# Optimization experiments

Hardware: AMD Instinct MI355X
Metric: run time of the kernel (lower is better)

The kernel has to match this reference:

```python
import jax, jax.numpy as jnp
import numpy as np

# dimensions
N = 50000    # nodes
E = 600000   # edges
NS = 64      # scalar (0e) channels of node features
NV = 32      # vector (1o) channels of node features
A = 16       # node attr channels (16x0e)
R = 8        # edge embedding dim (radial basis, 8x0e)
H = 8        # fc_hidden_size
AVG_NB = 12.0  # avg_num_neighbors
# gate layout: NS scalars (silu) + NV gate scalars (sigmoid) gating NV vectors
GS = NS + NV  # 96 scalar channels before gate
NW = NS + NS + NV + NV  # 192 per-edge TP weights (paths: s*Y0->0e, s*Y1->1o, v*Y0->1o, v.Y1->0e)


def setup_inputs() -> dict:
    key = jax.random.key(0)
    ks = jax.random.split(key, 20)
    d = {
        'node_s': jax.random.normal(ks[0], (N, NS), jnp.float32),
        'node_v': jax.random.normal(ks[1], (N, NV, 3), jnp.float32),
        'node_attrs': jax.random.normal(ks[2], (N, A), jnp.float32),
        'edge_emb': jax.random.uniform(ks[3], (E, R), jnp.float32),
        'edge_sh0': jnp.ones((E, 1), jnp.float32),
        'edge_sh1': jax.random.normal(ks[4], (E, 3), jnp.float32),
        'edge_index': jax.random.randint(ks[5], (2, E), 0, N),
        # linear_1 on node feats (per-irrep channel mixing)
        'W1s': jax.random.normal(ks[6], (NS, NS), jnp.float32),
        'W1v': jax.random.normal(ks[7], (NV, NV), jnp.float32),
        # radial MLP producing per-edge TP weights
        'Wm1': jax.random.normal(ks[8], (R, H), jnp.float32),
        'Wm2': jax.random.normal(ks[9], (H, NW), jnp.float32),
        # linear_2: TP out (96x0e+96x1o) -> pre-gate (96x0e+32x1o)
        'W2s': jax.random.normal(ks[10], (GS, GS), jnp.float32),
        'W2v': jax.random.normal(ks[11], (NS + NV, NV), jnp.float32),
        # update UVU TP internal weights (msg x attrs)
        'Wt0': jax.random.normal(ks[12], (NS, A), jnp.float32),
        'Wt1': jax.random.normal(ks[13], (NV, A), jnp.float32),
        # linear_3
        'W3s': jax.random.normal(ks[14], (NS, GS), jnp.float32),
        'W3v': jax.random.normal(ks[15], (NV, NV), jnp.float32),
        # self connection: FullyConnectedTensorProduct(node_feats, attrs -> pre-gate)
        'Wsc0': jax.random.normal(ks[16], (NS, A, GS), jnp.float32),
        'Wsc1': jax.random.normal(ks[17], (NV, A, NV), jnp.float32),
    }
    return d


def _gate(s_all, v):
    # s_all: [.., GS]; first NS scalars -> silu, last NV -> sigmoid gates for vectors
    scal = jax.nn.silu(s_all[..., :NS])
    gates = jax.nn.sigmoid(s_all[..., NS:])
    return scal, v * gates[..., None]


def reference(node_s, node_v, node_attrs, edge_emb, edge_sh0, edge_sh1, edge_index,
              W1s, W1v, Wm1, Wm2, W2s, W2v, Wt0, Wt1, W3s, W3v, Wsc0, Wsc1):
    src, dst = edge_index[0], edge_index[1]

    # ---- message ----
    s1 = (node_s @ W1s) / jnp.sqrt(jnp.float32(NS))                       # [N,NS]
    v1 = jnp.einsum('nuc,uv->nvc', node_v, W1v) / jnp.sqrt(jnp.float32(NV))
    ss = s1[src]   # [E,NS]
    vv = v1[src]   # [E,NV,3]

    # per-edge TP weights from radial MLP
    w = jax.nn.silu(edge_emb @ Wm1) @ Wm2                                 # [E,NW]
    w0a, w1a, w1b, w0b = jnp.split(w, [NS, 2 * NS, 2 * NS + NV], axis=1)

    # UVU tensor product with SH edge attrs (lmax=1)
    t0a = w0a * ss * edge_sh0                                             # [E,NS] 0e
    t0b = w0b * jnp.einsum('euc,ec->eu', vv, edge_sh1)                    # [E,NV] 0e
    t1a = w1a[:, :, None] * ss[:, :, None] * edge_sh1[:, None, :]         # [E,NS,3] 1o
    t1b = w1b[:, :, None] * vv * edge_sh0[:, :, None]                     # [E,NV,3] 1o
    tp_s = jnp.concatenate([t0a, t0b], axis=1)                            # [E,96]
    tp_v = jnp.concatenate([t1a, t1b], axis=1)                            # [E,96,3]

    m_s = (tp_s @ W2s) / jnp.sqrt(jnp.float32(GS))                        # [E,GS]
    m_v = jnp.einsum('euc,uv->evc', tp_v, W2v) / jnp.sqrt(jnp.float32(NS + NV))  # [E,NV,3]
    msg_s, msg_v = _gate(m_s, m_v)                                        # [E,NS], [E,NV,3]

    # ---- update ----
    agg_s = jax.ops.segment_sum(msg_s, dst, num_segments=N) / jnp.sqrt(jnp.float32(AVG_NB))
    agg_v = jax.ops.segment_sum(msg_v, dst, num_segments=N) / jnp.sqrt(jnp.float32(AVG_NB))

    u0 = jnp.einsum('nu,na,ua->nu', agg_s, node_attrs, Wt0) / jnp.sqrt(jnp.float32(A))
    u1 = jnp.einsum('nuc,na,ua->nuc', agg_v, node_attrs, Wt1) / jnp.sqrt(jnp.float32(A))

    f_s = (u0 @ W3s) / jnp.sqrt(jnp.float32(NS))                          # [N,GS]
    f_v = jnp.einsum('nuc,uv->nvc', u1, W3v) / jnp.sqrt(jnp.float32(NV))  # [N,NV,3]

    # self connection (fully connected TP with scalar attrs)
    sc_s = jnp.einsum('nu,na,uav->nv', node_s, node_attrs, Wsc0) / jnp.sqrt(jnp.float32(NS * A))
    sc_v = jnp.einsum('nuc,na,uaw->nwc', node_v, node_attrs, Wsc1) / jnp.sqrt(jnp.float32(NV * A))
    f_s = f_s + sc_s
    f_v = f_v + sc_v

    out_s, out_v = _gate(f_s, f_v)                                        # [N,NS], [N,NV,3]
    return jnp.concatenate([out_s, out_v.reshape(N, NV * 3)], axis=1)     # [N,160]
```

## Files before the change

### kernel.cpp

```cpp
#include <hip/hip_runtime.h>
#include <math.h>
#include <stdint.h>

#define N 50000
#define E 600000
#define EPB 16
#define LDK 104

typedef __attribute__((ext_vector_type(8))) short short8;
typedef __attribute__((ext_vector_type(4))) float float4v;

__device__ __forceinline__ float silu_f(float x) { return x / (1.f + __expf(-x)); }
__device__ __forceinline__ float sigm_f(float x) { return 1.f / (1.f + __expf(-x)); }
__device__ __forceinline__ unsigned short f2bf(float f) {
  unsigned u = __float_as_uint(f);
  u += 0x7fff + ((u >> 16) & 1);
  return (unsigned short)(u >> 16);
}
__device__ __forceinline__ float bf2f(unsigned short u) {
  return __uint_as_float(((unsigned)u) << 16);
}

__global__ void k_hist(const int* __restrict__ eidx, int* __restrict__ counts) {
  int e = blockIdx.x * 256 + threadIdx.x;
  if (e < E) atomicAdd(&counts[eidx[E + e]], 1);
}

__global__ __launch_bounds__(1024)
void k_scan(const int* __restrict__ counts, int* __restrict__ row_ptr) {
  __shared__ int ssum[1024];
  const int t = threadIdx.x;
  const int CH = 49;
  int lo = t * CH, hi = min(lo + CH, N);
  int s = 0;
  for (int i = lo; i < hi; i++) s += counts[i];
  ssum[t] = s;
  __syncthreads();
  for (int off = 1; off < 1024; off <<= 1) {
    int v = (t >= off) ? ssum[t - off] : 0;
    __syncthreads();
    ssum[t] += v;
    __syncthreads();
  }
  int run = (t == 0) ? 0 : ssum[t - 1];
  for (int i = lo; i < hi; i++) { row_ptr[i] = run; run += counts[i]; }
  if (t == 1023) row_ptr[N] = ssum[1023];
}

__global__ void k_scatter(const int* __restrict__ eidx, const int* __restrict__ row_ptr,
                          int* __restrict__ woff, int* __restrict__ perm) {
  int e = blockIdx.x * 256 + threadIdx.x;
  if (e < E) {
    int d = eidx[E + e];
    int p = atomicAdd(&woff[d], 1);
    perm[row_ptr[d] + p] = e;
  }
}

__global__ __launch_bounds__(256)
void k_init(const float* __restrict__ Wsc0, const float* __restrict__ W3s,
            const float* __restrict__ Wsc1, const float* __restrict__ W3v,
            const float* __restrict__ W2s, const float* __restrict__ W2v,
            unsigned short* __restrict__ BT, unsigned short* __restrict__ B2T,
            unsigned short* __restrict__ w2sTg, unsigned short* __restrict__ w2vTg,
            const float* __restrict__ node_s, const float* __restrict__ node_v,
            const float* __restrict__ W1s, const float* __restrict__ W1v,
            float* __restrict__ s1, float* __restrict__ v1,
            int* __restrict__ cnt, float* __restrict__ aggs) {
  __shared__ float w1s[64 * 64];
  __shared__ float w1v[32 * 32];
  const int b = blockIdx.x, t = threadIdx.x;
  const float isq96 = 0.10206207261596575f;

  if (b < 528) {
    int i = b * 256 + t;
    if (i < 96 * 1088) {
      int j = i / 1088, k = i % 1088;
      float v;
      if (k < 1024) v = Wsc0[(size_t)k * 96 + j] * 0.03125f;
      else          v = W3s[(size_t)(k - 1024) * 96 + j] * 0.125f;
      BT[i] = f2bf(v);
    } else if (i < 96 * 1088 + 32 * 576) {
      int i2 = i - 96 * 1088;
      int w = i2 / 576, k = i2 % 576;
      float v = 0.f;
      if (k < 512)      v = Wsc1[(size_t)k * 32 + w] * 0.04419417382415922f;
      else if (k < 544) v = W3v[(size_t)(k - 512) * 32 + w] * 0.17677669529663689f;
      B2T[i2] = f2bf(v);
    } else if (i < 96 * 1088 + 32 * 576 + 96 * 96) {
      int i3 = i - (96 * 1088 + 32 * 576);
      int j = i3 / 96, k = i3 % 96;
      w2sTg[i3] = f2bf(W2s[(size_t)k * 96 + j] * isq96);
    } else {
      int i4 = i - (96 * 1088 + 32 * 576 + 96 * 96);
      if (i4 < 32 * 96) {
        int v = i4 / 96, u = i4 % 96;
        w2vTg[i4] = f2bf(W2v[(size_t)u * 32 + v] * isq96);
      }
    }
  } else if (b < 1552) {
    for (int i = t; i < 64 * 64; i += 256) w1s[i] = W1s[i];
    for (int i = t; i < 32 * 32; i += 256) w1v[i] = W1v[i];
    __syncthreads();
    const float is_ns = 0.125f;
    const float is_nv = 0.17677669529663689f;
    int gtid = (b - 528) * 256 + t;
    const int stride = 1024 * 256;
    for (int i = gtid; i < N * 160; i += stride) {
      int n = i / 160, ch = i % 160;
      if (ch < 64) {
        const float* row = node_s + n * 64;
        float acc = 0.f;
#pragma unroll
        for (int u = 0; u < 64; u++) acc += row[u] * w1s[u * 64 + ch];
        s1[n * 64 + ch] = acc * is_ns;
      } else {
        int p = ch - 64, v = p / 3, c = p % 3;
        const float* row = node_v + n * 96;
        float acc = 0.f;
#pragma unroll
        for (int u = 0; u < 32; u++) acc += row[u * 3 + c] * w1v[u * 32 + v];
        v1[n * 96 + p] = acc * is_nv;
      }
    }
  } else if (b < 1943) {
    if (cnt) {
      int idx = (b - 1552) * 256 + t;
      if (idx < 2 * N) cnt[idx] = 0;
    }
  } else {
    float4v* a4 = (float4v*)aggs;
    const int tot = N * 160 / 4;
    const float4v z = {0.f, 0.f, 0.f, 0.f};
    for (int i = (b - 1943) * 256 + t; i < tot; i += 2000 * 256) a4[i] = z;
  }
}

template<int STORE>
__global__ __launch_bounds__(256, 4)
void k_msg(const float* __restrict__ s1, const float* __restrict__ v1,
           const float* __restrict__ emb, const float* __restrict__ sh0g,
           const float* __restrict__ sh1g, const int* __restrict__ eidx,
           const int* __restrict__ perm,
           const float* __restrict__ Wm1, const float* __restrict__ Wm2,
           const unsigned short* __restrict__ w2sTg, const unsigned short* __restrict__ w2vTg,
           float* __restrict__ aggs, float* __restrict__ aggv) {
  __shared__ float wm2s[192 * 9];
  __shared__ float wm1s[64];
  __shared__ unsigned short tps[EPB * LDK];
  __shared__ unsigned short tpv[EPB * 3 * LDK];
  __shared__ float gat[EPB][33];
  __shared__ float msL[EPB][65];
  __shared__ float mvL[EPB][97];
  __shared__ float hb[EPB][8];
  __shared__ float sh1b[EPB][4];
  __shared__ float sh0b[EPB];
  __shared__ int ssrc[EPB];
  __shared__ int sdst[EPB];

  const int t = threadIdx.x;
  const int wave = t >> 6, lane = t & 63;
  const int lm = lane & 15, quad = lane >> 4;
  const int subc = t & 15;

  for (int i = t; i < 192 * 8; i += 256) {
    int h = i / 192, c = i % 192;
    wm2s[c * 9 + h] = Wm2[i];
  }
  if (t < 64) wm1s[t] = Wm1[t];

  short8 b1fr[2][3], b2fr[3];
  {
    const int nt0 = wave;
    const int nt1 = (wave + 4 < 6) ? wave + 4 : wave;
    const int nv2 = wave & 1;
#pragma unroll
    for (int kk = 0; kk < 3; kk++) {
      b1fr[0][kk] = *(const short8*)&w2sTg[(nt0 * 16 + lm) * 96 + kk * 32 + quad * 8];
      b1fr[1][kk] = *(const short8*)&w2sTg[(nt1 * 16 + lm) * 96 + kk * 32 + quad * 8];
      b2fr[kk]    = *(const short8*)&w2vTg[(nv2 * 16 + lm) * 96 + kk * 32 + quad * 8];
    }
  }
  __syncthreads();

  for (int pass = blockIdx.x; pass < E / EPB; pass += gridDim.x) {
    const int ebase = pass * EPB;
    __syncthreads();
    if (t < EPB) {
      const int e = STORE ? perm[ebase + t] : (ebase + t);
      ssrc[t] = eidx[e];
      sdst[t] = eidx[E + e];
      sh0b[t] = sh0g[e];
    } else if (t >= 64 && t < 64 + EPB * 3) {
      int i = t - 64;
      const int el = i / 3, c = i % 3;
      const int e = STORE ? perm[ebase + el] : (ebase + el);
      sh1b[el][c] = sh1g[e * 3 + c];
    } else if (t >= 128) {
      int i = t - 128, el = i >> 3, sub = i & 7;
      const int e = STORE ? perm[ebase + el] : (ebase + el);
      float acc = 0.f;
#pragma unroll
      for (int r = 0; r < 8; r++) acc += emb[e * 8 + r] * wm1s[r * 8 + sub];
      hb[el][sub] = silu_f(acc);
    }
    __syncthreads();
    {
      const int el = t >> 4, sub = subc;
      const int src = ssrc[el];
      const float s0v = sh0b[el];
      const float x0 = sh1b[el][0], x1 = sh1b[el][1], x2 = sh1b[el][2];
      float hr[8];
#pragma unroll
      for (int h = 0; h < 8; h++) hr[h] = hb[el][h];
      const float4v ss = *(const float4v*)&s1[(size_t)src * 64 + sub * 4];
      unsigned short tsv[4], tvv[3][4];
#pragma unroll
      for (int i = 0; i < 4; i++) {
        float w0a = 0.f, w1a = 0.f;
#pragma unroll
        for (int h = 0; h < 8; h++) {
          w0a += hr[h] * wm2s[(sub * 4 + i) * 9 + h];
          w1a += hr[h] * wm2s[(64 + sub * 4 + i) * 9 + h];
        }
        const float ssu = ss[i];
        tsv[i] = f2bf(w0a * ssu * s0v);
        const float base = w1a * ssu;
        tvv[0][i] = f2bf(base * x0);
        tvv[1][i] = f2bf(base * x1);
        tvv[2][i] = f2bf(base * x2);
      }
      *(uint2*)&tps[el * LDK + sub * 4] = *(uint2*)tsv;
#pragma unroll
      for (int c = 0; c < 3; c++)
        *(uint2*)&tpv[(el * 3 + c) * LDK + sub * 4] = *(uint2*)tvv[c];
      const float2* vp = (const float2*)&v1[(size_t)src * 96 + sub * 6];
      const float2 va = vp[0], vb = vp[1], vc = vp[2];
      const float v6[6] = {va.x, va.y, vb.x, vb.y, vc.x, vc.y};
      unsigned short ts2[2], tv2[3][2];
#pragma unroll
      for (int i2 = 0; i2 < 2; i2++) {
        float w1b = 0.f, w0b = 0.f;
#pragma unroll
        for (int h = 0; h < 8; h++) {
          w1b += hr[h] * wm2s[(128 + sub * 2 + i2) * 9 + h];
          w0b += hr[h] * wm2s[(160 + sub * 2 + i2) * 9 + h];
        }
        const float vx = v6[i2 * 3 + 0], vy = v6[i2 * 3 + 1], vz = v6[i2 * 3 + 2];
        ts2[i2] = f2bf(w0b * (vx * x0 + vy * x1 + vz * x2));
        tv2[0][i2] = f2bf(w1b * vx * s0v);
        tv2[1][i2] = f2bf(w1b * vy * s0v);
        tv2[2][i2] = f2bf(w1b * vz * s0v);
      }
      *(unsigned*)&tps[el * LDK + 64 + sub * 2] = *(unsigned*)ts2;
#pragma unroll
      for (int c = 0; c < 3; c++)
        *(unsigned*)&tpv[(el * 3 + c) * LDK + 64 + sub * 2] = *(unsigned*)tv2[c];
    }
    __syncthreads();
    if (STORE) {
      short8 afr[3];
#pragma unroll
      for (int kk = 0; kk < 3; kk++)
        afr[kk] = *(const short8*)&tps[lm * LDK + kk * 32 + quad * 8];
#pragma unroll
      for (int tt = 0; tt < 3; tt++) {
        const int id = wave + tt * 4;
        float4v acc = {0.f, 0.f, 0.f, 0.f};
        if (id < 6) {
          const int t2 = id >> 2;
#pragma unroll
          for (int kk = 0; kk < 3; kk++)
            acc = __builtin_amdgcn_mfma_f32_16x16x32_bf16(afr[kk], b1fr[t2][kk], acc, 0, 0, 0);
          const int j = id * 16 + lm;
#pragma unroll
          for (int reg = 0; reg < 4; reg++) {
            const int e = quad * 4 + reg;
            const float val = acc[reg];
            if (j < 64) msL[e][j] = silu_f(val);
            else        gat[e][j - 64] = sigm_f(val);
          }
        } else {
          const int g2 = id - 6;
          const int mt = g2 >> 1, nt2 = g2 & 1;
#pragma unroll
          for (int kk = 0; kk < 3; kk++) {
            short8 a = *(const short8*)&tpv[(mt * 16 + lm) * LDK + kk * 32 + quad * 8];
            acc = __builtin_amdgcn_mfma_f32_16x16x32_bf16(a, b2fr[kk], acc, 0, 0, 0);
          }
          const int v = nt2 * 16 + lm;
#pragma unroll
          for (int reg = 0; reg < 4; reg++) {
            const int r = mt * 16 + quad * 4 + reg;
            const int e = (r * 171) >> 9, c = r - 3 * e;
            mvL[e][v * 3 + c] = acc[reg];
          }
        }
      }
      __syncthreads();
      if (t < 160) {
        const int col = t - 64;
        const int gv = (col * 171) >> 9;
        float acc = 0.f;
        int cur = sdst[0];
        for (int s2 = 0; s2 < EPB; s2++) {
          const int d = sdst[s2];
          const float val = (t < 64) ? msL[s2][t] : mvL[s2][col] * gat[s2][gv];
          if (d != cur) {
            if (t < 64) atomicAdd(&aggs[(size_t)cur * 64 + t], acc);
            else        atomicAdd(&aggv[(size_t)cur * 96 + col], acc);
            acc = 0.f; cur = d;
          }
          acc += val;
        }
        if (t < 64) atomicAdd(&aggs[(size_t)cur * 64 + t], acc);
        else        atomicAdd(&aggv[(size_t)cur * 96 + col], acc);
      }
    } else {
      {
        short8 afr[3];
#pragma unroll
        for (int kk = 0; kk < 3; kk++)
          afr[kk] = *(const short8*)&tps[lm * LDK + kk * 32 + quad * 8];
#pragma unroll
        for (int t2 = 0; t2 < 2; t2++) {
          const int nt = wave + t2 * 4;
          if (nt < 6) {
            float4v acc = {0.f, 0.f, 0.f, 0.f};
#pragma unroll
            for (int kk = 0; kk < 3; kk++)
              acc = __builtin_amdgcn_mfma_f32_16x16x32_bf16(afr[kk], b1fr[t2][kk], acc, 0, 0, 0);
            const int j = nt * 16 + lm;
#pragma unroll
            for (int reg = 0; reg < 4; reg++) {
              const int e = quad * 4 + reg;
              const float val = acc[reg];
              if (j < 64) atomicAdd(&aggs[(size_t)sdst[e] * 64 + j], silu_f(val));
              else        gat[e][j - 64] = sigm_f(val);
            }
          }
        }
      }
      __syncthreads();
#pragma unroll
      for (int t2 = 0; t2 < 2; t2++) {
        const int tile = wave + t2 * 4;
        if (tile < 6) {
          const int mt = tile >> 1, nt2 = tile & 1;
          float4v acc = {0.f, 0.f, 0.f, 0.f};
#pragma unroll
          for (int kk = 0; kk < 3; kk++) {
            short8 a = *(const short8*)&tpv[(mt * 16 + lm) * LDK + kk * 32 + quad * 8];
            acc = __builtin_amdgcn_mfma_f32_16x16x32_bf16(a, b2fr[kk], acc, 0, 0, 0);
          }
          const int v = nt2 * 16 + lm;
#pragma unroll
          for (int reg = 0; reg < 4; reg++) {
            const int r = mt * 16 + quad * 4 + reg;
            const int e = (r * 171) >> 9, c = r - 3 * e;
            atomicAdd(&aggv[(size_t)sdst[e] * 96 + v * 3 + c], acc[reg] * gat[e][v]);
          }
        }
      }
    }
  }
}

__global__ __launch_bounds__(256, 4)
void k_c1(const float* __restrict__ node_s, const float* __restrict__ attrs,
          const float* __restrict__ aggs, const float* __restrict__ Wt0,
          const unsigned short* __restrict__ BT,
          float* __restrict__ out, float* __restrict__ gates) {
  __shared__ float s_row[32][65];
  __shared__ float attr[32][16];
  __shared__ float t0[32][65];
  __shared__ float wt0[1024];
  const int t = threadIdx.x;
  const int wave = t >> 6, lane = t & 63, lm = lane & 15, quad = lane >> 4;
  const int nbase = blockIdx.x * 32;

  for (int i = t; i < 1024; i += 256) wt0[i] = Wt0[i];
  for (int i = t; i < 2048; i += 256) {
    int nl = i >> 6, u = i & 63, n = nbase + nl;
    s_row[nl][u] = (n < N) ? node_s[(size_t)n * 64 + u] : 0.f;
    t0[nl][u]    = (n < N) ? aggs[(size_t)n * 64 + u] : 0.f;
  }
  for (int i = t; i < 512; i += 256) {
    int nl = i >> 4, a = i & 15, n = nbase + nl;
    attr[nl][a] = (n < N) ? attrs[(size_t)n * 16 + a] : 0.f;
  }
  __syncthreads();
  for (int i = t; i < 2048; i += 256) {
    int nl = i >> 6, u = i & 63;
    float d0 = 0.f;
#pragma unroll
    for (int a = 0; a < 16; a++) d0 += attr[nl][a] * wt0[u * 16 + a];
    t0[nl][u] *= d0 * 0.07216878364870322f;
  }
  __syncthreads();

  const int a0 = (quad & 1) * 8;
  float aA0[8], aA1[8];
#pragma unroll
  for (int i = 0; i < 8; i++) {
    aA0[i] = attr[lm][a0 + i];
    aA1[i] = attr[16 + lm][a0 + i];
  }

  float4v acc[3] = {{0,0,0,0},{0,0,0,0},{0,0,0,0}};
  int mts[3], nts[3];
#pragma unroll
  for (int tt = 0; tt < 3; tt++) {
    const int tile = wave + tt * 4;
    mts[tt] = tile / 6;
    nts[tt] = tile % 6;
  }

  for (int kc = 0; kc < 17; kc++) {
#pragma unroll
    for (int ks = 0; ks < 2; ks++) {
      unsigned short e0[8], e1[8];
      if (kc < 16) {
        const int u = kc * 4 + ks * 2 + (quad >> 1);
        const float s0v = s_row[lm][u];
        const float s1v = s_row[16 + lm][u];
#pragma unroll
        for (int i = 0; i < 8; i++) {
          e0[i] = f2bf(s0v * aA0[i]);
          e1[i] = f2bf(s1v * aA1[i]);
        }
      } else {
        const int c0 = ks * 32 + quad * 8;
#pragma unroll
        for (int i = 0; i < 8; i++) {
          e0[i] = f2bf(t0[lm][c0 + i]);
          e1[i] = f2bf(t0[16 + lm][c0 + i]);
        }
      }
      const short8 am0 = *(const short8*)e0;
      const short8 am1 = *(const short8*)e1;
#pragma unroll
      for (int tt = 0; tt < 3; tt++) {
        short8 b = *(const short8*)&BT[(size_t)(nts[tt] * 16 + lm) * 1088 + kc * 64 + ks * 32 + quad * 8];
        acc[tt] = __builtin_amdgcn_mfma_f32_16x16x32_bf16(mts[tt] ? am1 : am0, b, acc[tt], 0, 0, 0);
      }
    }
  }
#pragma unroll
  for (int tt = 0; tt < 3; tt++) {
    const int j = nts[tt] * 16 + lm;
#pragma unroll
    for (int reg = 0; reg < 4; reg++) {
      const int m = mts[tt] * 16 + quad * 4 + reg;
      const int n = nbase + m;
      if (n < N) {
        const float val = acc[tt][reg];
        if (j < 64) out[(size_t)n * 160 + j] = silu_f(val);
        else        gates[(size_t)n * 32 + (j - 64)] = sigm_f(val);
      }
    }
  }
}

__global__ __launch_bounds__(256, 4)
void k_c2(const float* __restrict__ node_v, const float* __restrict__ attrs,
          const float* __restrict__ aggv, const float* __restrict__ Wt1,
          const unsigned short* __restrict__ B2T, const float* __restrict__ gts,
          float* __restrict__ out) {
  __shared__ float nvs[32][97];
  __shared__ float t1s[32][97];
  __shared__ float attr[32][16];
  __shared__ float wt1[512];
  const int t = threadIdx.x;
  const int wave = t >> 6, lane = t & 63, lm = lane & 15, quad = lane >> 4;
  const int nbase = blockIdx.x * 32;

  for (int i = t; i < 512; i += 256) wt1[i] = Wt1[i];
  for (int i = t; i < 32 * 96; i += 256) {
    int nl = i / 96, rr = i % 96, n = nbase + nl;
    nvs[nl][rr] = (n < N) ? node_v[(size_t)n * 96 + rr] : 0.f;
    t1s[nl][rr] = (n < N) ? aggv[(size_t)n * 96 + rr] : 0.f;
  }
  for (int i = t; i < 512; i += 256) {
    int nl = i >> 4, a = i & 15, n = nbase + nl;
    attr[nl][a] = (n < N) ? attrs[(size_t)n * 16 + a] : 0.f;
  }
  __syncthreads();
  for (int i = t; i < 1024; i += 256) {
    int nl = i >> 5, u = i & 31;
    float d1 = 0.f;
#pragma unroll
    for (int a = 0; a < 16; a++) d1 += attr[nl][a] * wt1[u * 16 + a];
    d1 *= 0.07216878364870322f;
    t1s[nl][u * 3 + 0] *= d1; t1s[nl][u * 3 + 1] *= d1; t1s[nl][u * 3 + 2] *= d1;
  }
  __syncthreads();

  int nls[3], cs[3], nts[3], mts[3];
#pragma unroll
  for (int tt = 0; tt < 3; tt++) {
    const int tile = wave + tt * 4;
    mts[tt] = tile >> 1;
    nts[tt] = tile & 1;
    const int row = mts[tt] * 16 + lm;
    nls[tt] = (row * 171) >> 9;
    cs[tt]  = row - 3 * nls[tt];
  }
  const int a0 = (quad & 1) * 8;
  float aA[3][8];
#pragma unroll
  for (int tt = 0; tt < 3; tt++)
#pragma unroll
    for (int i = 0; i < 8; i++) aA[tt][i] = attr[nls[tt]][a0 + i];

  float4v acc[3] = {{0,0,0,0},{0,0,0,0},{0,0,0,0}};

  for (int kc = 0; kc < 9; kc++) {
#pragma unroll
    for (int ks = 0; ks < 2; ks++) {
      if (kc == 8 && ks == 1) continue;
#pragma unroll
      for (int tt = 0; tt < 3; tt++) {
        unsigned short ev[8];
        if (kc < 8) {
          const int u = kc * 4 + ks * 2 + (quad >> 1);
          const float vv = nvs[nls[tt]][u * 3 + cs[tt]];
#pragma unroll
          for (int i = 0; i < 8; i++) ev[i] = f2bf(vv * aA[tt][i]);
        } else {
#pragma unroll
          for (int i = 0; i < 8; i++) ev[i] = f2bf(t1s[nls[tt]][(quad * 8 + i) * 3 + cs[tt]]);
        }
        const short8 a = *(const short8*)ev;
        short8 b = *(const short8*)&B2T[(size_t)(nts[tt] * 16 + lm) * 576 + kc * 64 + ks * 32 + quad * 8];
        acc[tt] = __builtin_amdgcn_mfma_f32_16x16x32_bf16(a, b, acc[tt], 0, 0, 0);
      }
    }
  }
#pragma unroll
  for (int tt = 0; tt < 3; tt++) {
    const int w = nts[tt] * 16 + lm;
#pragma unroll
    for (int reg = 0; reg < 4; reg++) {
      const int row = mts[tt] * 16 + quad * 4 + reg;
      const int nl = (row * 171) >> 9, c = row - 3 * nl;
      const int n = nbase + nl;
      if (n < N)
        out[(size_t)n * 160 + 64 + w * 3 + c] = acc[tt][reg] * gts[(size_t)n * 32 + w];
    }
  }
}

extern "C" void kernel_launch(void* const* d_in, const int* in_sizes, int n_in,
                              void* d_out, int out_size, void* d_ws, size_t ws_size,
                              hipStream_t stream) {
  const float* node_s = (const float*)d_in[0];
  const float* node_v = (const float*)d_in[1];
  const float* attrs  = (const float*)d_in[2];
  const float* emb    = (const float*)d_in[3];
  const float* sh0    = (const float*)d_in[4];
  const float* sh1    = (const float*)d_in[5];
  const int*   eidx   = (const int*)d_in[6];
  const float* W1s    = (const float*)d_in[7];
  const float* W1v    = (const float*)d_in[8];
  const float* Wm1    = (const float*)d_in[9];
  const float* Wm2    = (const float*)d_in[10];
  const float* W2s    = (const float*)d_in[11];
  const float* W2v    = (const float*)d_in[12];
  const float* Wt0    = (const float*)d_in[13];
  const float* Wt1    = (const float*)d_in[14];
  const float* W3s    = (const float*)d_in[15];
  const float* W3v    = (const float*)d_in[16];
  const float* Wsc0   = (const float*)d_in[17];
  const float* Wsc1   = (const float*)d_in[18];

  char* p = (char*)d_ws;
  float* s1  = (float*)p;  p += (size_t)N * 64 * 4;
  float* v1f = (float*)p;  p += (size_t)N * 96 * 4;
  float* gts = (float*)p;  p += (size_t)N * 32 * 4;
  unsigned short* BT    = (unsigned short*)p;  p += (size_t)96 * 1088 * 2;
  unsigned short* B2T   = (unsigned short*)p;  p += (size_t)32 * 576 * 2;
  unsigned short* w2sTg = (unsigned short*)p;  p += (size_t)96 * 96 * 2;
  unsigned short* w2vTg = (unsigned short*)p;  p += (size_t)32 * 96 * 2;
  char* pmode = p;
  size_t base = (size_t)(pmode - (char*)d_ws);
  size_t need_store = base + ((size_t)N + 1) * 4 + (size_t)N * 4 + (size_t)N * 4
                    + (size_t)E * 4 + 16 + (size_t)N * 160 * 4;
  const bool store = (ws_size >= need_store);

  if (store) {
    int* rowp = (int*)pmode;
    int* cnt  = rowp + (N + 1);
    int* woff = cnt + N;
    int* perm = woff + N;
    float* aggs = (float*)(((uintptr_t)(perm + E) + 15) & ~(uintptr_t)15);
    float* aggv = aggs + (size_t)N * 64;
    k_init<<<3943, 256, 0, stream>>>(Wsc0, W3s, Wsc1, W3v, W2s, W2v, BT, B2T, w2sTg, w2vTg,
                                     node_s, node_v, W1s, W1v, s1, v1f, cnt, aggs);
    k_hist<<<(E + 255) / 256, 256, 0, stream>>>(eidx, cnt);
    k_scan<<<1, 1024, 0, stream>>>(cnt, rowp);
    k_scatter<<<(E + 255) / 256, 256, 0, stream>>>(eidx, rowp, woff, perm);
    k_msg<1><<<1024, 256, 0, stream>>>(s1, v1f, emb, sh0, sh1, eidx, perm, Wm1, Wm2,
                                       w2sTg, w2vTg, aggs, aggv);
    k_c1<<<1563, 256, 0, stream>>>(node_s, attrs, aggs, Wt0, BT, (float*)d_out, gts);
    k_c2<<<1563, 256, 0, stream>>>(node_v, attrs, aggv, Wt1, B2T, gts, (float*)d_out);
  } else {
    float* aggs = (float*)pmode;
    float* aggv = aggs + (size_t)N * 64;
    k_init<<<3943, 256, 0, stream>>>(Wsc0, W3s, Wsc1, W3v, W2s, W2v, BT, B2T, w2sTg, w2vTg,
                                     node_s, node_v, W1s, W1v, s1, v1f, nullptr, aggs);
    k_msg<0><<<1024, 256, 0, stream>>>(s1, v1f, emb, sh0, sh1, eidx, nullptr, Wm1, Wm2,
                                       w2sTg, w2vTg, aggs, aggv);
    k_c1<<<1563, 256, 0, stream>>>(node_s, attrs, aggs, Wt0, BT, (float*)d_out, gts);
    k_c2<<<1563, 256, 0, stream>>>(node_v, attrs, aggv, Wt1, B2T, gts, (float*)d_out);
  }
}
```

Baseline: 679.7 us.

## Store linear_1 outputs as bf16 and fuse scalar/vector update kernels

Measured after the change: 678.3 us. Within noise of the previous version (-0.2%).

```diff
diff --git a/kernel.cpp b/kernel.cpp
--- a/kernel.cpp
+++ b/kernel.cpp
@@ -20,6 +20,8 @@
 __device__ __forceinline__ float bf2f(unsigned short u) {
   return __uint_as_float(((unsigned)u) << 16);
 }
+__device__ __forceinline__ float bf2f_lo(unsigned u) { return __uint_as_float(u << 16); }
+__device__ __forceinline__ float bf2f_hi(unsigned u) { return __uint_as_float(u & 0xffff0000u); }
 
 __global__ void k_hist(const int* __restrict__ eidx, int* __restrict__ counts) {
   int e = blockIdx.x * 256 + threadIdx.x;
@@ -65,7 +67,7 @@
             unsigned short* __restrict__ w2sTg, unsigned short* __restrict__ w2vTg,
             const float* __restrict__ node_s, const float* __restrict__ node_v,
             const float* __restrict__ W1s, const float* __restrict__ W1v,
-            float* __restrict__ s1, float* __restrict__ v1,
+            unsigned short* __restrict__ s1b, unsigned short* __restrict__ v1b,
             int* __restrict__ cnt, float* __restrict__ aggs) {
   __shared__ float w1s[64 * 64];
   __shared__ float w1v[32 * 32];
@@ -113,14 +115,14 @@
         float acc = 0.f;
 #pragma unroll
         for (int u = 0; u < 64; u++) acc += row[u] * w1s[u * 64 + ch];
-        s1[n * 64 + ch] = acc * is_ns;
+        s1b[n * 64 + ch] = f2bf(acc * is_ns);
       } else {
         int p = ch - 64, v = p / 3, c = p % 3;
         const float* row = node_v + n * 96;
         float acc = 0.f;
 #pragma unroll
         for (int u = 0; u < 32; u++) acc += row[u * 3 + c] * w1v[u * 32 + v];
-        v1[n * 96 + p] = acc * is_nv;
+        v1b[n * 96 + p] = f2bf(acc * is_nv);
       }
     }
   } else if (b < 1943) {
@@ -138,7 +140,7 @@
 
 template<int STORE>
 __global__ __launch_bounds__(256, 4)
-void k_msg(const float* __restrict__ s1, const float* __restrict__ v1,
+void k_msg(const unsigned short* __restrict__ s1b, const unsigned short* __restrict__ v1b,
            const float* __restrict__ emb, const float* __restrict__ sh0g,
            const float* __restrict__ sh1g, const int* __restrict__ eidx,
            const int* __restrict__ perm,
@@ -213,7 +215,9 @@
       float hr[8];
 #pragma unroll
       for (int h = 0; h < 8; h++) hr[h] = hb[el][h];
-      const float4v ss = *(const float4v*)&s1[(size_t)src * 64 + sub * 4];
+      const unsigned* sp = (const unsigned*)(s1b + (size_t)src * 64 + sub * 4);
+      const unsigned sw0 = sp[0], sw1 = sp[1];
+      const float ssv[4] = { bf2f_lo(sw0), bf2f_hi(sw0), bf2f_lo(sw1), bf2f_hi(sw1) };
       unsigned short tsv[4], tvv[3][4];
 #pragma unroll
       for (int i = 0; i < 4; i++) {
@@ -223,7 +227,7 @@
           w0a += hr[h] * wm2s[(sub * 4 + i) * 9 + h];
           w1a += hr[h] * wm2s[(64 + sub * 4 + i) * 9 + h];
         }
-        const float ssu = ss[i];
+        const float ssu = ssv[i];
         tsv[i] = f2bf(w0a * ssu * s0v);
         const float base = w1a * ssu;
         tvv[0][i] = f2bf(base * x0);
@@ -234,9 +238,10 @@
 #pragma unroll
       for (int c = 0; c < 3; c++)
         *(uint2*)&tpv[(el * 3 + c) * LDK + sub * 4] = *(uint2*)tvv[c];
-      const float2* vp = (const float2*)&v1[(size_t)src * 96 + sub * 6];
-      const float2 va = vp[0], vb = vp[1], vc = vp[2];
-      const float v6[6] = {va.x, va.y, vb.x, vb.y, vc.x, vc.y};
+      const unsigned* vp = (const unsigned*)(v1b + (size_t)src * 96 + sub * 6);
+      const unsigned vw0 = vp[0], vw1 = vp[1], vw2 = vp[2];
+      const float v6[6] = { bf2f_lo(vw0), bf2f_hi(vw0), bf2f_lo(vw1),
+                            bf2f_hi(vw1), bf2f_lo(vw2), bf2f_hi(vw2) };
       unsigned short ts2[2], tv2[3][2];
 #pragma unroll
       for (int i2 = 0; i2 < 2; i2++) {
@@ -367,186 +372,184 @@
 }
 
 __global__ __launch_bounds__(256, 4)
-void k_c1(const float* __restrict__ node_s, const float* __restrict__ attrs,
-          const float* __restrict__ aggs, const float* __restrict__ Wt0,
-          const unsigned short* __restrict__ BT,
-          float* __restrict__ out, float* __restrict__ gates) {
-  __shared__ float s_row[32][65];
+void k_cd(const float* __restrict__ node_s, const float* __restrict__ node_v,
+          const float* __restrict__ attrs,
+          const float* __restrict__ aggs, const float* __restrict__ aggv,
+          const float* __restrict__ Wt0, const float* __restrict__ Wt1,
+          const unsigned short* __restrict__ BT, const unsigned short* __restrict__ B2T,
+          float* __restrict__ out) {
+  __shared__ float bufA[2 * 32 * 97];
   __shared__ float attr[32][16];
-  __shared__ float t0[32][65];
-  __shared__ float wt0[1024];
+  __shared__ float wtb[1024];
+  __shared__ float gatesL[32][33];
   const int t = threadIdx.x;
   const int wave = t >> 6, lane = t & 63, lm = lane & 15, quad = lane >> 4;
   const int nbase = blockIdx.x * 32;
 
-  for (int i = t; i < 1024; i += 256) wt0[i] = Wt0[i];
-  for (int i = t; i < 2048; i += 256) {
-    int nl = i >> 6, u = i & 63, n = nbase + nl;
-    s_row[nl][u] = (n < N) ? node_s[(size_t)n * 64 + u] : 0.f;
-    t0[nl][u]    = (n < N) ? aggs[(size_t)n * 64 + u] : 0.f;
-  }
-  for (int i = t; i < 512; i += 256) {
-    int nl = i >> 4, a = i & 15, n = nbase + nl;
-    attr[nl][a] = (n < N) ? attrs[(size_t)n * 16 + a] : 0.f;
+  {
+    float* s_row = bufA;
+    float* t0    = bufA + 32 * 97;
+
+    for (int i = t; i < 1024; i += 256) wtb[i] = Wt0[i];
+    for (int i = t; i < 2048; i += 256) {
+      int nl = i >> 6, u = i & 63, n = nbase + nl;
+      s_row[nl * 97 + u] = (n < N) ? node_s[(size_t)n * 64 + u] : 0.f;
+      t0[nl * 97 + u]    = (n < N) ? aggs[(size_t)n * 64 + u] : 0.f;
+    }
+    for (int i = t; i < 512; i += 256) {
+      int nl = i >> 4, a = i & 15, n = nbase + nl;
+      attr[nl][a] = (n < N) ? attrs[(size_t)n * 16 + a] : 0.f;
+    }
+    __syncthreads();
+    for (int i = t; i < 2048; i += 256) {
+      int nl = i >> 6, u = i & 63;
+      float d0 = 0.f;
+#pragma unroll
+      for (int a = 0; a < 16; a++) d0 += attr[nl][a] * wtb[u * 16 + a];
+      t0[nl * 97 + u] *= d0 * 0.07216878364870322f;
+    }
+    __syncthreads();
+
+    const int a0 = (quad & 1) * 8;
+    float aA0[8], aA1[8];
+#pragma unroll
+    for (int i = 0; i < 8; i++) {
+      aA0[i] = attr[lm][a0 + i];
+      aA1[i] = attr[16 + lm][a0 + i];
+    }
+
+    float4v acc[3] = {{0,0,0,0},{0,0,0,0},{0,0,0,0}};
+    int mts[3], nts[3];
+#pragma unroll
+    for (int tt = 0; tt < 3; tt++) {
+      const int tile = wave + tt * 4;
+      mts[tt] = tile / 6;
+      nts[tt] = tile % 6;
+    }
+
+    for (int kc = 0; kc < 17; kc++) {
+#pragma unroll
+      for (int ks = 0; ks < 2; ks++) {
+        unsigned short e0[8], e1[8];
+        if (kc < 16) {
+          const int u = kc * 4 + ks * 2 + (quad >> 1);
+          const float s0v = s_row[lm * 97 + u];
+          const float s1v = s_row[(16 + lm) * 97 + u];
+#pragma unroll
+          for (int i = 0; i < 8; i++) {
+            e0[i] = f2bf(s0v * aA0[i]);
+            e1[i] = f2bf(s1v * aA1[i]);
+          }
+        } else {
+          const int c0 = ks * 32 + quad * 8;
+#pragma unroll
+          for (int i = 0; i < 8; i++) {
+            e0[i] = f2bf(t0[lm * 97 + c0 + i]);
+            e1[i] = f2bf(t0[(16 + lm) * 97 + c0 + i]);
+          }
+        }
+        const short8 am0 = *(const short8*)e0;
+        const short8 am1 = *(const short8*)e1;
+#pragma unroll
+        for (int tt = 0; tt < 3; tt++) {
+          short8 b = *(const short8*)&BT[(size_t)(nts[tt] * 16 + lm) * 1088 + kc * 64 + ks * 32 + quad * 8];
+          acc[tt] = __builtin_amdgcn_mfma_f32_16x16x32_bf16(mts[tt] ? am1 : am0, b, acc[tt], 0, 0, 0);
+        }
+      }
+    }
+#pragma unroll
+    for (int tt = 0; tt < 3; tt++) {
+      const int j = nts[tt] * 16 + lm;
+#pragma unroll
+      for (int reg = 0; reg < 4; reg++) {
+        const int m = mts[tt] * 16 + quad * 4 + reg;
+        const int n = nbase + m;
+        const float val = acc[tt][reg];
+        if (j < 64) {
+          if (n < N) out[(size_t)n * 160 + j] = silu_f(val);
+        } else {
+          gatesL[m][j - 64] = sigm_f(val);
+        }
+      }
+    }
   }
   __syncthreads();
-  for (int i = t; i < 2048; i += 256) {
-    int nl = i >> 6, u = i & 63;
-    float d0 = 0.f;
-#pragma unroll
-    for (int a = 0; a < 16; a++) d0 += attr[nl][a] * wt0[u * 16 + a];
-    t0[nl][u] *= d0 * 0.07216878364870322f;
-  }
-  __syncthreads();
-
-  const int a0 = (quad & 1) * 8;
-  float aA0[8], aA1[8];
-#pragma unroll
-  for (int i = 0; i < 8; i++) {
-    aA0[i] = attr[lm][a0 + i];
-    aA1[i] = attr[16 + lm][a0 + i];
-  }
-
-  float4v acc[3] = {{0,0,0,0},{0,0,0,0},{0,0,0,0}};
-  int mts[3], nts[3];
-#pragma unroll
-  for (int tt = 0; tt < 3; tt++) {
-    const int tile = wave + tt * 4;
-    mts[tt] = tile / 6;
-    nts[tt] = tile % 6;
-  }
-
-  for (int kc = 0; kc < 17; kc++) {
-#pragma unroll
-    for (int ks = 0; ks < 2; ks++) {
-      unsigned short e0[8], e1[8];
-      if (kc < 16) {
-        const int u = kc * 4 + ks * 2 + (quad >> 1);
-        const float s0v = s_row[lm][u];
-        const float s1v = s_row[16 + lm][u];
-#pragma unroll
-        for (int i = 0; i < 8; i++) {
-          e0[i] = f2bf(s0v * aA0[i]);
-          e1[i] = f2bf(s1v * aA1[i]);
-        }
-      } else {
-        const int c0 = ks * 32 + quad * 8;
-#pragma unroll
-        for (int i = 0; i < 8; i++) {
-          e0[i] = f2bf(t0[lm][c0 + i]);
-          e1[i] = f2bf(t0[16 + lm][c0 + i]);
-        }
-      }
-      const short8 am0 = *(const short8*)e0;
-      const short8 am1 = *(const short8*)e1;
-#pragma unroll
-      for (int tt = 0; tt < 3; tt++) {
-        short8 b = *(const short8*)&BT[(size_t)(nts[tt] * 16 + lm) * 1088 + kc * 64 + ks * 32 + quad * 8];
-        acc[tt] = __builtin_amdgcn_mfma_f32_16x16x32_bf16(mts[tt] ? am1 : am0, b, acc[tt], 0, 0, 0);
-      }
-    }
-  }
-#pragma unroll
-  for (int tt = 0; tt < 3; tt++) {
-    const int j = nts[tt] * 16 + lm;
-#pragma unroll
-    for (int reg = 0; reg < 4; reg++) {
-      const int m = mts[tt] * 16 + quad * 4 + reg;
-      const int n = nbase + m;
-      if (n < N) {
-        const float val = acc[tt][reg];
-        if (j < 64) out[(size_t)n * 160 + j] = silu_f(val);
-        else        gates[(size_t)n * 32 + (j - 64)] = sigm_f(val);
-      }
-    }
-  }
-}
-
-__global__ __launch_bounds__(256, 4)
-void k_c2(const float* __restrict__ node_v, const float* __restrict__ attrs,
-          const float* __restrict__ aggv, const float* __restrict__ Wt1,
-          const unsigned short* __restrict__ B2T, const float* __restrict__ gts,
-          float* __restrict__ out) {
-  __shared__ float nvs[32][97];
-  __shared__ float t1s[32][97];
-  __shared__ float attr[32][16];
-  __shared__ float wt1[512];
-  const int t = threadIdx.x;
-  const int wave = t >> 6, lane = t & 63, lm = lane & 15, quad = lane >> 4;
-  const int nbase = blockIdx.x * 32;
-
-  for (int i = t; i < 512; i += 256) wt1[i] = Wt1[i];
-  for (int i = t; i < 32 * 96; i += 256) {
-    int nl = i / 96, rr = i % 96, n = nbase + nl;
-    nvs[nl][rr] = (n < N) ? node_v[(size_t)n * 96 + rr] : 0.f;
-    t1s[nl][rr] = (n < N) ? aggv[(size_t)n * 96 + rr] : 0.f;
-  }
-  for (int i = t; i < 512; i += 256) {
-    int nl = i >> 4, a = i & 15, n = nbase + nl;
-    attr[nl][a] = (n < N) ? attrs[(size_t)n * 16 + a] : 0.f;
-  }
-  __syncthreads();
-  for (int i = t; i < 1024; i += 256) {
-    int nl = i >> 5, u = i & 31;
-    float d1 = 0.f;
-#pragma unroll
-    for (int a = 0; a < 16; a++) d1 += attr[nl][a] * wt1[u * 16 + a];
-    d1 *= 0.07216878364870322f;
-    t1s[nl][u * 3 + 0] *= d1; t1s[nl][u * 3 + 1] *= d1; t1s[nl][u * 3 + 2] *= d1;
-  }
-  __syncthreads();
-
-  int nls[3], cs[3], nts[3], mts[3];
-#pragma unroll
-  for (int tt = 0; tt < 3; tt++) {
-    const int tile = wave + tt * 4;
-    mts[tt] = tile >> 1;
-    nts[tt] = tile & 1;
-    const int row = mts[tt] * 16 + lm;
-    nls[tt] = (row * 171) >> 9;
-    cs[tt]  = row - 3 * nls[tt];
-  }
-  const int a0 = (quad & 1) * 8;
-  float aA[3][8];
-#pragma unroll
-  for (int tt = 0; tt < 3; tt++)
-#pragma unroll
-    for (int i = 0; i < 8; i++) aA[tt][i] = attr[nls[tt]][a0 + i];
-
-  float4v acc[3] = {{0,0,0,0},{0,0,0,0},{0,0,0,0}};
-
-  for (int kc = 0; kc < 9; kc++) {
-#pragma unroll
-    for (int ks = 0; ks < 2; ks++) {
-      if (kc == 8 && ks == 1) continue;
-#pragma unroll
-      for (int tt = 0; tt < 3; tt++) {
-        unsigned short ev[8];
-        if (kc < 8) {
-          const int u = kc * 4 + ks * 2 + (quad >> 1);
-          const float vv = nvs[nls[tt]][u * 3 + cs[tt]];
-#pragma unroll
-          for (int i = 0; i < 8; i++) ev[i] = f2bf(vv * aA[tt][i]);
-        } else {
-#pragma unroll
-          for (int i = 0; i < 8; i++) ev[i] = f2bf(t1s[nls[tt]][(quad * 8 + i) * 3 + cs[tt]]);
-        }
-        const short8 a = *(const short8*)ev;
-        short8 b = *(const short8*)&B2T[(size_t)(nts[tt] * 16 + lm) * 576 + kc * 64 + ks * 32 + quad * 8];
-        acc[tt] = __builtin_amdgcn_mfma_f32_16x16x32_bf16(a, b, acc[tt], 0, 0, 0);
-      }
-    }
-  }
-#pragma unroll
-  for (int tt = 0; tt < 3; tt++) {
-    const int w = nts[tt] * 16 + lm;
-#pragma unroll
-    for (int reg = 0; reg < 4; reg++) {
-      const int row = mts[tt] * 16 + quad * 4 + reg;
-      const int nl = (row * 171) >> 9, c = row - 3 * nl;
-      const int n = nbase + nl;
-      if (n < N)
-        out[(size_t)n * 160 + 64 + w * 3 + c] = acc[tt][reg] * gts[(size_t)n * 32 + w];
+
+  {
+    float* nvs = bufA;
+    float* t1s = bufA + 32 * 97;
+
+    for (int i = t; i < 512; i += 256) wtb[i] = Wt1[i];
+    for (int i = t; i < 32 * 96; i += 256) {
+      int nl = i / 96, rr = i % 96, n = nbase + nl;
+      nvs[nl * 97 + rr] = (n < N) ? node_v[(size_t)n * 96 + rr] : 0.f;
+      t1s[nl * 97 + rr] = (n < N) ? aggv[(size_t)n * 96 + rr] : 0.f;
+    }
+    __syncthreads();
+    for (int i = t; i < 1024; i += 256) {
+      int nl = i >> 5, u = i & 31;
+      float d1 = 0.f;
+#pragma unroll
+      for (int a = 0; a < 16; a++) d1 += attr[nl][a] * wtb[u * 16 + a];
+      d1 *= 0.07216878364870322f;
+      t1s[nl * 97 + u * 3 + 0] *= d1;
+      t1s[nl * 97 + u * 3 + 1] *= d1;
+      t1s[nl * 97 + u * 3 + 2] *= d1;
+    }
+    __syncthreads();
+
+    int nls[3], cs[3], nts[3], mts[3];
+#pragma unroll
+    for (int tt = 0; tt < 3; tt++) {
+      const int tile = wave + tt * 4;
+      mts[tt] = tile >> 1;
+      nts[tt] = tile & 1;
+      const int row = mts[tt] * 16 + lm;
+      nls[tt] = (row * 171) >> 9;
+      cs[tt]  = row - 3 * nls[tt];
+    }
+    const int a0 = (quad & 1) * 8;
+    float aA[3][8];
+#pragma unroll
+    for (int tt = 0; tt < 3; tt++)
+#pragma unroll
+      for (int i = 0; i < 8; i++) aA[tt][i] = attr[nls[tt]][a0 + i];
+
+    float4v acc[3] = {{0,0,0,0},{0,0,0,0},{0,0,0,0}};
+
+    for (int kc = 0; kc < 9; kc++) {
+#pragma unroll
+      for (int ks = 0; ks < 2; ks++) {
+        if (kc == 8 && ks == 1) continue;
+#pragma unroll
+        for (int tt = 0; tt < 3; tt++) {
+          unsigned short ev[8];
+          if (kc < 8) {
+            const int u = kc * 4 + ks * 2 + (quad >> 1);
+            const float vv = nvs[nls[tt] * 97 + u * 3 + cs[tt]];
+#pragma unroll
+            for (int i = 0; i < 8; i++) ev[i] = f2bf(vv * aA[tt][i]);
+          } else {
+#pragma unroll
+            for (int i = 0; i < 8; i++) ev[i] = f2bf(t1s[nls[tt] * 97 + (quad * 8 + i) * 3 + cs[tt]]);
+          }
+          const short8 a = *(const short8*)ev;
+          short8 b = *(const short8*)&B2T[(size_t)(nts[tt] * 16 + lm) * 576 + kc * 64 + ks * 32 + quad * 8];
+          acc[tt] = __builtin_amdgcn_mfma_f32_16x16x32_bf16(a, b, acc[tt], 0, 0, 0);
+        }
+      }
+    }
+#pragma unroll
+    for (int tt = 0; tt < 3; tt++) {
+      const int w = nts[tt] * 16 + lm;
+#pragma unroll
+      for (int reg = 0; reg < 4; reg++) {
+        const int row = mts[tt] * 16 + quad * 4 + reg;
+        const int nl = (row * 171) >> 9, c = row - 3 * nl;
+        const int n = nbase + nl;
+        if (n < N)
+          out[(size_t)n * 160 + 64 + w * 3 + c] = acc[tt][reg] * gatesL[nl][w];
+      }
     }
   }
 }
@@ -575,9 +578,8 @@
   const float* Wsc1   = (const float*)d_in[18];
 
   char* p = (char*)d_ws;
-  float* s1  = (float*)p;  p += (size_t)N * 64 * 4;
-  float* v1f = (float*)p;  p += (size_t)N * 96 * 4;
-  float* gts = (float*)p;  p += (size_t)N * 32 * 4;
+  unsigned short* s1b = (unsigned short*)p;  p += (size_t)N * 64 * 2;
+  unsigned short* v1b = (unsigned short*)p;  p += (size_t)N * 96 * 2;
   unsigned short* BT    = (unsigned short*)p;  p += (size_t)96 * 1088 * 2;
   unsigned short* B2T   = (unsigned short*)p;  p += (size_t)32 * 576 * 2;
   unsigned short* w2sTg = (unsigned short*)p;  p += (size_t)96 * 96 * 2;
@@ -596,22 +598,22 @@
     float* aggs = (float*)(((uintptr_t)(perm + E) + 15) & ~(uintptr_t)15);
     float* aggv = aggs + (size_t)N * 64;
     k_init<<<3943, 256, 0, stream>>>(Wsc0, W3s, Wsc1, W3v, W2s, W2v, BT, B2T, w2sTg, w2vTg,
-                                     node_s, node_v, W1s, W1v, s1, v1f, cnt, aggs);
+                                     node_s, node_v, W1s, W1v, s1b, v1b, cnt, aggs);
     k_hist<<<(E + 255) / 256, 256, 0, stream>>>(eidx, cnt);
     k_scan<<<1, 1024, 0, stream>>>(cnt, rowp);
     k_scatter<<<(E + 255) / 256, 256, 0, stream>>>(eidx, rowp, woff, perm);
-    k_msg<1><<<1024, 256, 0, stream>>>(s1, v1f, emb, sh0, sh1, eidx, perm, Wm1, Wm2,
+    k_msg<1><<<1024, 256, 0, stream>>>(s1b, v1b, emb, sh0, sh1, eidx, perm, Wm1, Wm2,
                                        w2sTg, w2vTg, aggs, aggv);
-    k_c1<<<1563, 256, 0, stream>>>(node_s, attrs, aggs, Wt0, BT, (float*)d_out, gts);
-    k_c2<<<1563, 256, 0, stream>>>(node_v, attrs, aggv, Wt1, B2T, gts, (float*)d_out);
+    k_cd<<<1563, 256, 0, stream>>>(node_s, node_v, attrs, aggs, aggv, Wt0, Wt1,
+                                   BT, B2T, (float*)d_out);
   } else {
-    float* aggs = (float*)pmode;
+    float* aggs = (float*)(((uintptr_t)pmode + 15) & ~(uintptr_t)15);
     float* aggv = aggs + (size_t)N * 64;
     k_init<<<3943, 256, 0, stream>>>(Wsc0, W3s, Wsc1, W3v, W2s, W2v, BT, B2T, w2sTg, w2vTg,
-                                     node_s, node_v, W1s, W1v, s1, v1f, nullptr, aggs);
-    k_msg<0><<<1024, 256, 0, stream>>>(s1, v1f, emb, sh0, sh1, eidx, nullptr, Wm1, Wm2,
+                                     node_s, node_v, W1s, W1v, s1b, v1b, nullptr, aggs);
+    k_msg<0><<<1024, 256, 0, stream>>>(s1b, v1b, emb, sh0, sh1, eidx, nullptr, Wm1, Wm2,
                                        w2sTg, w2vTg, aggs, aggv);
-    k_c1<<<1563, 256, 0, stream>>>(node_s, attrs, aggs, Wt0, BT, (float*)d_out, gts);
-    k_c2<<<1563, 256, 0, stream>>>(node_v, attrs, aggv, Wt1, B2T, gts, (float*)d_out);
-  }
-}
+    k_cd<<<1563, 256, 0, stream>>>(node_s, node_v, attrs, aggs, aggv, Wt0, Wt1,
+                                   BT, B2T, (float*)d_out);
+  }
+}
```
